# Optimization experiments

Measured on AMD Instinct MI355X. Metric: run time of the kernel, lower is better.

Reference implementation:

```python
import jax, jax.numpy as jnp
import numpy as np


def _lstm_cell(x, h, c, W_ih, b_ih, W_hh, b_hh):
    # PyTorch gate order: i, f, g, o
    gates = x @ W_ih.T + b_ih + h @ W_hh.T + b_hh
    i, f, g, o = jnp.split(gates, 4, axis=-1)
    c = jax.nn.sigmoid(f) * c + jax.nn.sigmoid(i) * jnp.tanh(g)
    h = jax.nn.sigmoid(o) * jnp.tanh(c)
    return h, c


def setup_inputs() -> dict:
    key = jax.random.key(0)
    ks = jax.random.split(key, 12)
    B, CR, PR = 8192, 168, 24
    E, I, H = 20, 3, 40  # embedding_size, input_size, hidden_size
    s = 0.1
    return {
        "z1": jax.random.normal(ks[0], (B, CR, 1), jnp.float32),
        "xc": jax.random.normal(ks[1], (B, CR + PR, I), jnp.float32),
        "W_emb": jax.random.normal(ks[2], (E, 1), jnp.float32) * s,
        "b_emb": jax.random.normal(ks[3], (E,), jnp.float32) * s,
        "W_ih": jax.random.normal(ks[4], (4 * H, E + I), jnp.float32) * s,
        "b_ih": jax.random.normal(ks[5], (4 * H,), jnp.float32) * s,
        "W_hh": jax.random.normal(ks[6], (4 * H, H), jnp.float32) * s,
        "b_hh": jax.random.normal(ks[7], (4 * H,), jnp.float32) * s,
        "W_mu": jax.random.normal(ks[8], (1, H), jnp.float32) * s,
        "b_mu": jax.random.normal(ks[9], (1,), jnp.float32) * s,
        "W_sig": jax.random.normal(ks[10], (1, H), jnp.float32) * s,
        "b_sig": jax.random.normal(ks[11], (1,), jnp.float32) * s,
        "conditioning_range": 168,
        "prediction_range": 24,
    }


def reference(z1, xc, W_emb, b_emb, W_ih, b_ih, W_hh, b_hh, W_mu, b_mu, W_sig, b_sig, conditioning_range, prediction_range):
    B = z1.shape[0]
    H = W_hh.shape[1]
    v = jnp.mean(z1, axis=1, keepdims=True) + 1.0  # [B,1,1] scale factor
    v2 = v[:, 0, :]                                # [B,1]

    # ---- conditioning phase: t = 1 .. CR-1 ----
    emb_cond = (z1[:, : conditioning_range - 1, :] / v) @ W_emb.T + b_emb  # [B,CR-1,E]
    xs = jnp.concatenate([emb_cond, xc[:, 1:conditioning_range, :]], axis=-1)
    xs = jnp.swapaxes(xs, 0, 1)  # [T,B,E+I]
    h0 = jnp.zeros((B, H), z1.dtype)
    c0 = jnp.zeros((B, H), z1.dtype)

    def cond_step(carry, x_t):
        h, c = carry
        h, c = _lstm_cell(x_t, h, c, W_ih, b_ih, W_hh, b_hh)
        return (h, c), None

    (h, c), _ = jax.lax.scan(cond_step, (h0, c0), xs)

    eps = jax.random.normal(jax.random.key(42), (prediction_range, B, 1), z1.dtype)
    xc_pred = jnp.swapaxes(
        xc[:, conditioning_range: conditioning_range + prediction_range, :], 0, 1
    )  # [PR,B,I]

    def pred_step(carry, inp):
        h, c, y = carry
        x_t, e_t = inp
        emb = (y / v2) @ W_emb.T + b_emb                       # [B,E]
        h, c = _lstm_cell(jnp.concatenate([emb, x_t], axis=-1), h, c, W_ih, b_ih, W_hh, b_hh)
        mu = h @ W_mu.T + b_mu                                 # [B,1]
        sigma = jax.nn.softplus(h @ W_sig.T + b_sig)           # [B,1]
        y = jax.lax.stop_gradient(mu + sigma * e_t)            # Normal.sample (no grad)
        return (h, c, y), (y * v2, mu * v2, sigma * v2)

    y0 = z1[:, -1, :]  # [B,1]
    _, (outs, mus, sigmas) = jax.lax.scan(pred_step, (h, c, y0), (xc_pred, eps))

    outputs = jnp.swapaxes(outs, 0, 1)[..., :]   # [B,PR,1]
    mus = jnp.swapaxes(mus, 0, 1)
    sigmas = jnp.swapaxes(sigmas, 0, 1)
    return outputs, mus, sigmas
```

## Files before the change

### kernel.cpp

```cpp
#include <hip/hip_runtime.h>

#define B_TOTAL   8192
#define CR_LEN    168
#define PR_LEN    24
#define HID       40
#define ROWS      6
#define NTHREADS  256
#define OUT_STRIDE (B_TOTAL * PR_LEN)

__device__ __forceinline__ float fast_rcp(float x) { return __builtin_amdgcn_rcpf(x); }

__device__ __forceinline__ float sigmoid_f(float x) {
    return fast_rcp(1.0f + __expf(-x));
}

__device__ __forceinline__ float tanh_f(float x) {
    float ax = fabsf(x);
    float e  = __expf(-2.0f * ax);
    float r  = (1.0f - e) * fast_rcp(1.0f + e);
    return copysignf(r, x);
}

__device__ __forceinline__ unsigned rotl32(unsigned x, int d) {
    return (x << d) | (x >> (32 - d));
}

__device__ __forceinline__ void threefry2x32(unsigned k0, unsigned k1,
                                             unsigned c0, unsigned c1,
                                             unsigned& o0, unsigned& o1) {
    const unsigned k2 = 0x1BD11BDAu ^ k0 ^ k1;
    unsigned x0 = c0 + k0, x1 = c1 + k1;
#define TF_R(rr) { x0 += x1; x1 = rotl32(x1, (rr)); x1 ^= x0; }
    TF_R(13) TF_R(15) TF_R(26) TF_R(6)  x0 += k1; x1 += k2 + 1u;
    TF_R(17) TF_R(29) TF_R(16) TF_R(24) x0 += k2; x1 += k0 + 2u;
    TF_R(13) TF_R(15) TF_R(26) TF_R(6)  x0 += k0; x1 += k1 + 3u;
    TF_R(17) TF_R(29) TF_R(16) TF_R(24) x0 += k1; x1 += k2 + 4u;
    TF_R(13) TF_R(15) TF_R(26) TF_R(6)  x0 += k2; x1 += k0 + 5u;
#undef TF_R
    o0 = x0; o1 = x1;
}

__device__ __forceinline__ float erfinv_f(float x) {
    float w = -__logf(fmaf(-x, x, 1.0f));
    float p;
    if (w < 5.0f) {
        w -= 2.5f;
        p = 2.81022636e-08f;
        p = fmaf(p, w, 3.43273939e-07f);
        p = fmaf(p, w, -3.5233877e-06f);
        p = fmaf(p, w, -4.39150654e-06f);
        p = fmaf(p, w, 0.00021858087f);
        p = fmaf(p, w, -0.00125372503f);
        p = fmaf(p, w, -0.00417768164f);
        p = fmaf(p, w, 0.246640727f);
        p = fmaf(p, w, 1.50140941f);
    } else {
        w = sqrtf(w) - 3.0f;
        p = -0.000200214257f;
        p = fmaf(p, w, 0.000100950558f);
        p = fmaf(p, w, 0.00134934322f);
        p = fmaf(p, w, -0.00367342844f);
        p = fmaf(p, w, 0.00573950773f);
        p = fmaf(p, w, -0.0076224613f);
        p = fmaf(p, w, 0.00943887047f);
        p = fmaf(p, w, 1.00167406f);
        p = fmaf(p, w, 2.83297682f);
    }
    return p * x;
}

__device__ __forceinline__ float kat_poison() {
    float poison = 0.0f;
    unsigned o0, o1;
    threefry2x32(0u, 0u, 0u, 0u, o0, o1);
    bool ok1 = (o0 == 0x6b200159u) && (o1 == 0x99ba4efeu);
    threefry2x32(0xFFFFFFFFu, 0xFFFFFFFFu, 0xFFFFFFFFu, 0xFFFFFFFFu, o0, o1);
    bool ok2 = (o0 == 0x1cb996fcu) && (o1 == 0xbb002be7u);
    if (!(ok1 && ok2)) poison += 4096.0f;
    threefry2x32(0x13198a2eu, 0x03707344u, 0x243f6a88u, 0x85a308d3u, o0, o1);
    bool ok3 = (o0 == 0xc4923a9cu) && (o1 == 0x483df7a0u);
    if (!ok3) poison += 8192.0f;
    return poison;
}

#define KEEPQ(q) asm volatile("" : "+v"((q).x), "+v"((q).y), "+v"((q).z), "+v"((q).w))

#define DOT4(acc, w4, h4) \
    acc = fmaf((w4).x, (h4).x, acc); acc = fmaf((w4).y, (h4).y, acc); \
    acc = fmaf((w4).z, (h4).z, acc); acc = fmaf((w4).w, (h4).w, acc);

#define LSTM_STEP(z1n, xa, xb, xv, hptr) do {                                  \
    float a0 = fmaf(fA0, (z1n), fC0); float a1 = fmaf(fA1, (z1n), fC1);        \
    float a2 = fmaf(fA2, (z1n), fC2); float a3 = fmaf(fA3, (z1n), fC3);        \
    a0 = fmaf(fp00, (xa), a0); a1 = fmaf(fp01, (xa), a1);                      \
    a2 = fmaf(fp02, (xa), a2); a3 = fmaf(fp03, (xa), a3);                      \
    a0 = fmaf(fp10, (xb), a0); a1 = fmaf(fp11, (xb), a1);                      \
    a2 = fmaf(fp12, (xb), a2); a3 = fmaf(fp13, (xb), a3);                      \
    a0 = fmaf(fp20, (xv), a0); a1 = fmaf(fp21, (xv), a1);                      \
    a2 = fmaf(fp22, (xv), a2); a3 = fmaf(fp23, (xv), a3);                      \
    float4 h4;                                                                 \
    h4 = ((const float4*)(hptr))[0];                                           \
    DOT4(a0, wA0, h4) DOT4(a1, wB0, h4) DOT4(a2, wC0, h4) DOT4(a3, wD0, h4)    \
    h4 = ((const float4*)(hptr))[1];                                           \
    DOT4(a0, wA1, h4) DOT4(a1, wB1, h4) DOT4(a2, wC1, h4) DOT4(a3, wD1, h4)    \
    h4 = ((const float4*)(hptr))[2];                                           \
    DOT4(a0, wA2, h4) DOT4(a1, wB2, h4) DOT4(a2, wC2, h4) DOT4(a3, wD2, h4)    \
    h4 = ((const float4*)(hptr))[3];                                           \
    DOT4(a0, wA3, h4) DOT4(a1, wB3, h4) DOT4(a2, wC3, h4) DOT4(a3, wD3, h4)    \
    h4 = ((const float4*)(hptr))[4];                                           \
    DOT4(a0, wA4, h4) DOT4(a1, wB4, h4) DOT4(a2, wC4, h4) DOT4(a3, wD4, h4)    \
    h4 = ((const float4*)(hptr))[5];                                           \
    DOT4(a0, wA5, h4) DOT4(a1, wB5, h4) DOT4(a2, wC5, h4) DOT4(a3, wD5, h4)    \
    h4 = ((const float4*)(hptr))[6];                                           \
    DOT4(a0, wA6, h4) DOT4(a1, wB6, h4) DOT4(a2, wC6, h4) DOT4(a3, wD6, h4)    \
    h4 = ((const float4*)(hptr))[7];                                           \
    DOT4(a0, wA7, h4) DOT4(a1, wB7, h4) DOT4(a2, wC7, h4) DOT4(a3, wD7, h4)    \
    h4 = ((const float4*)(hptr))[8];                                           \
    DOT4(a0, wA8, h4) DOT4(a1, wB8, h4) DOT4(a2, wC8, h4) DOT4(a3, wD8, h4)    \
    h4 = ((const float4*)(hptr))[9];                                           \
    DOT4(a0, wA9, h4) DOT4(a1, wB9, h4) DOT4(a2, wC9, h4) DOT4(a3, wD9, h4)    \
    float gi = sigmoid_f(a0);                                                  \
    float gf = sigmoid_f(a1);                                                  \
    float gg = tanh_f(a2);                                                     \
    float go = sigmoid_f(a3);                                                  \
    c_st = fmaf(gf, c_st, gi * gg);                                            \
    h_st = go * tanh_f(c_st);                                                  \
} while (0)

#define LOADW(P, base)                                                         \
    float4 P##0 = pw[(base) + 0], P##1 = pw[(base) + 1],                       \
           P##2 = pw[(base) + 2], P##3 = pw[(base) + 3],                       \
           P##4 = pw[(base) + 4], P##5 = pw[(base) + 5],                       \
           P##6 = pw[(base) + 6], P##7 = pw[(base) + 7],                       \
           P##8 = pw[(base) + 8], P##9 = pw[(base) + 9];                       \
    KEEPQ(P##0); KEEPQ(P##1); KEEPQ(P##2); KEEPQ(P##3); KEEPQ(P##4);           \
    KEEPQ(P##5); KEEPQ(P##6); KEEPQ(P##7); KEEPQ(P##8); KEEPQ(P##9);

#define XCOEF(g, fAv, fCv, f0v, f1v, f2v) {                                    \
    const int row_ = (g) * HID + j;                                            \
    const float* wr_ = W_ih + row_ * 23;                                       \
    float a_ = 0.0f, cc_ = b_ih[row_] + b_hh[row_];                            \
    _Pragma("unroll")                                                          \
    for (int e = 0; e < 20; e++) {                                             \
        float wv_ = wr_[e];                                                    \
        a_  = fmaf(wv_, W_emb[e], a_);                                         \
        cc_ = fmaf(wv_, b_emb[e], cc_);                                        \
    }                                                                          \
    fAv = a_; fCv = cc_; f0v = wr_[20]; f1v = wr_[21]; f2v = wr_[22];          \
}

__launch_bounds__(NTHREADS, 1)
__global__ void deepar_kernel(const float* __restrict__ z1,
                              const float* __restrict__ xc,
                              const float* __restrict__ W_emb,
                              const float* __restrict__ b_emb,
                              const float* __restrict__ W_ih,
                              const float* __restrict__ b_ih,
                              const float* __restrict__ W_hh,
                              const float* __restrict__ b_hh,
                              const float* __restrict__ W_mu,
                              const float* __restrict__ b_mu,
                              const float* __restrict__ W_sig,
                              const float* __restrict__ b_sig,
                              float* __restrict__ out) {
    __shared__ __align__(16) float z1_s[ROWS][CR_LEN];
    __shared__ __align__(16) float xc_s[ROWS][(CR_LEN + PR_LEN) * 3];
    __shared__ __align__(16) float h_s[2][ROWS][HID];
    __shared__ float eps_s[ROWS][PR_LEN];
    __shared__ float y_s[ROWS];
    __shared__ __align__(16) float wmu_s[HID];
    __shared__ __align__(16) float wsg_s[HID];
    __shared__ float bmu_s, bsg_s;

    const int tid = threadIdx.x;
    const int r   = tid / HID;
    const int j   = tid % HID;
    const int b0  = blockIdx.x * ROWS;
    const int b   = b0 + r;
    const bool active = (r < ROWS) && (b < B_TOTAL);

    {
        int nrow = B_TOTAL - b0;
        if (nrow > ROWS) nrow = ROWS;
        if (nrow < 0) nrow = 0;
        const float4* s1 = (const float4*)(z1 + (size_t)b0 * CR_LEN);
        float4* d1 = (float4*)&z1_s[0][0];
        const int n1 = nrow * (CR_LEN / 4);
        for (int idx = tid; idx < n1; idx += NTHREADS) d1[idx] = s1[idx];
        const float4* s2 = (const float4*)(xc + (size_t)b0 * (CR_LEN + PR_LEN) * 3);
        float4* d2 = (float4*)&xc_s[0][0];
        const int n2 = nrow * ((CR_LEN + PR_LEN) * 3 / 4);
        for (int idx = tid; idx < n2; idx += NTHREADS) d2[idx] = s2[idx];
    }
    if (tid < HID)                 wmu_s[tid] = W_mu[tid];
    else if (tid < 2 * HID)        wsg_s[tid - HID] = W_sig[tid - HID];
    else if (tid == 2 * HID)       bmu_s = b_mu[0];
    else if (tid == 2 * HID + 1)   bsg_s = b_sig[0];

    const float4* pw = (const float4*)W_hh;
    LOADW(wA, (0 * HID + j) * 10)
    LOADW(wB, (1 * HID + j) * 10)
    LOADW(wC, (2 * HID + j) * 10)
    LOADW(wD, (3 * HID + j) * 10)

    float fA0, fA1, fA2, fA3, fC0, fC1, fC2, fC3;
    float fp00, fp01, fp02, fp03, fp10, fp11, fp12, fp13, fp20, fp21, fp22, fp23;
    XCOEF(0, fA0, fC0, fp00, fp10, fp20)
    XCOEF(1, fA1, fC1, fp01, fp11, fp21)
    XCOEF(2, fA2, fC2, fp02, fp12, fp22)
    XCOEF(3, fA3, fC3, fp03, fp13, fp23)

    __syncthreads();

    float v = 0.0f, inv_v = 0.0f;
    if (active) {
        float s = 0.0f;
#pragma unroll
        for (int q = 0; q < CR_LEN / 4; q++) {
            float4 zz = *(const float4*)&z1_s[r][4 * q];
            s += zz.x + zz.y + zz.z + zz.w;
        }
        v = s * (1.0f / (float)CR_LEN) + 1.0f;
        inv_v = 1.0f / v;
    }

    if (active && j < PR_LEN) {
        unsigned i = (unsigned)j * B_TOTAL + (unsigned)b;
        unsigned o0, o1;
        threefry2x32(0u, 42u, 0u, i, o0, o1);
        unsigned bits = o0 ^ o1;
        float f = __uint_as_float((bits >> 9) | 0x3F800000u) - 1.0f;
        const float lo = -0.99999994f;
        float u = fmaxf(lo, fmaf(f, 2.0f, lo));
        eps_s[r][j] = 1.41421356237f * erfinv_f(u);
    }

    if (active) { h_s[0][r][j] = 0.0f; }
    float c_st = 0.0f, h_st = 0.0f;
    __syncthreads();

    int cur = 0;

    for (int t = 0; t < CR_LEN - 1; t++) {
        if (active) {
            float z1n = z1_s[r][t] * inv_v;
            float xa = xc_s[r][3 * (t + 1) + 0];
            float xb = xc_s[r][3 * (t + 1) + 1];
            float xv = xc_s[r][3 * (t + 1) + 2];
            LSTM_STEP(z1n, xa, xb, xv, &h_s[cur][r][0]);
            h_s[cur ^ 1][r][j] = h_st;
        }
        __syncthreads();
        cur ^= 1;
    }

    if (active && j == 0) y_s[r] = z1_s[r][CR_LEN - 1];
    __syncthreads();

    for (int t = 0; t < PR_LEN; t++) {
        if (active) {
            float z1n = y_s[r] * inv_v;
            float xa = xc_s[r][3 * (CR_LEN + t) + 0];
            float xb = xc_s[r][3 * (CR_LEN + t) + 1];
            float xv = xc_s[r][3 * (CR_LEN + t) + 2];
            LSTM_STEP(z1n, xa, xb, xv, &h_s[cur][r][0]);
            h_s[cur ^ 1][r][j] = h_st;
        }
        __syncthreads();
        cur ^= 1;
        if (active && j == 0) {
            float mu = bmu_s, sp = bsg_s;
#pragma unroll
            for (int q = 0; q < 10; q++) {
                float4 h4 = *(const float4*)&h_s[cur][r][4 * q];
                float4 wm = *(const float4*)&wmu_s[4 * q];
                float4 ws = *(const float4*)&wsg_s[4 * q];
                mu = fmaf(wm.x, h4.x, mu); mu = fmaf(wm.y, h4.y, mu);
                mu = fmaf(wm.z, h4.z, mu); mu = fmaf(wm.w, h4.w, mu);
                sp = fmaf(ws.x, h4.x, sp); sp = fmaf(ws.y, h4.y, sp);
                sp = fmaf(ws.z, h4.z, sp); sp = fmaf(ws.w, h4.w, sp);
            }
            float sigma = fmaxf(sp, 0.0f) + log1pf(__expf(-fabsf(sp)));
            float y = fmaf(sigma, eps_s[r][t], mu);
            y_s[r] = y;
            const int ob = b * PR_LEN + t;
            float poison = (b == 0 && t == 0) ? kat_poison() : 0.0f;
            out[ob]                  = y * v + poison;
            out[OUT_STRIDE + ob]     = mu * v;
            out[2 * OUT_STRIDE + ob] = sigma * v;
        }
        __syncthreads();
    }
}

extern "C" void kernel_launch(void* const* d_in, const int* in_sizes, int n_in,
                              void* d_out, int out_size, void* d_ws, size_t ws_size,
                              hipStream_t stream) {
    const float* z1    = (const float*)d_in[0];
    const float* xc    = (const float*)d_in[1];
    const float* W_emb = (const float*)d_in[2];
    const float* b_emb = (const float*)d_in[3];
    const float* W_ih  = (const float*)d_in[4];
    const float* b_ih  = (const float*)d_in[5];
    const float* W_hh  = (const float*)d_in[6];
    const float* b_hh  = (const float*)d_in[7];
    const float* W_mu  = (const float*)d_in[8];
    const float* b_mu  = (const float*)d_in[9];
    const float* W_sig = (const float*)d_in[10];
    const float* b_sig = (const float*)d_in[11];
    float* out = (float*)d_out;

    dim3 grid((B_TOTAL + ROWS - 1) / ROWS);
    dim3 block(NTHREADS);
    deepar_kernel<<<grid, block, 0, stream>>>(z1, xc, W_emb, b_emb, W_ih, b_ih,
                                              W_hh, b_hh, W_mu, b_mu, W_sig, b_sig,
                                              out);
}
```

Measured before the change: 535.7 us.

## Split LSTM gates across two thread halves with shared-memory exchange

Each hidden unit's four gates are now computed by two threads, each owning two gates (i,f vs g,o), with g/o pre-activations exchanged through shared memory. Blocks shrink to 4 batch rows with 320 threads, so each thread holds half the recurrent weights and does half the dot-product work per step. The cost is an extra __syncthreads per timestep, more blocks, and partial-batch guards removed (relies on B divisible by 4).

Result: slower. 954.0 us (+78.1%).

```diff
diff --git a/kernel.cpp b/kernel.cpp
--- a/kernel.cpp
+++ b/kernel.cpp
@@ -4,8 +4,8 @@
 #define CR_LEN    168
 #define PR_LEN    24
 #define HID       40
-#define ROWS      6
-#define NTHREADS  256
+#define ROWS      4
+#define NTHREADS  320
 #define OUT_STRIDE (B_TOTAL * PR_LEN)
 
 __device__ __forceinline__ float fast_rcp(float x) { return __builtin_amdgcn_rcpf(x); }
@@ -89,44 +89,6 @@
     acc = fmaf((w4).x, (h4).x, acc); acc = fmaf((w4).y, (h4).y, acc); \
     acc = fmaf((w4).z, (h4).z, acc); acc = fmaf((w4).w, (h4).w, acc);
 
-#define LSTM_STEP(z1n, xa, xb, xv, hptr) do {                                  \
-    float a0 = fmaf(fA0, (z1n), fC0); float a1 = fmaf(fA1, (z1n), fC1);        \
-    float a2 = fmaf(fA2, (z1n), fC2); float a3 = fmaf(fA3, (z1n), fC3);        \
-    a0 = fmaf(fp00, (xa), a0); a1 = fmaf(fp01, (xa), a1);                      \
-    a2 = fmaf(fp02, (xa), a2); a3 = fmaf(fp03, (xa), a3);                      \
-    a0 = fmaf(fp10, (xb), a0); a1 = fmaf(fp11, (xb), a1);                      \
-    a2 = fmaf(fp12, (xb), a2); a3 = fmaf(fp13, (xb), a3);                      \
-    a0 = fmaf(fp20, (xv), a0); a1 = fmaf(fp21, (xv), a1);                      \
-    a2 = fmaf(fp22, (xv), a2); a3 = fmaf(fp23, (xv), a3);                      \
-    float4 h4;                                                                 \
-    h4 = ((const float4*)(hptr))[0];                                           \
-    DOT4(a0, wA0, h4) DOT4(a1, wB0, h4) DOT4(a2, wC0, h4) DOT4(a3, wD0, h4)    \
-    h4 = ((const float4*)(hptr))[1];                                           \
-    DOT4(a0, wA1, h4) DOT4(a1, wB1, h4) DOT4(a2, wC1, h4) DOT4(a3, wD1, h4)    \
-    h4 = ((const float4*)(hptr))[2];                                           \
-    DOT4(a0, wA2, h4) DOT4(a1, wB2, h4) DOT4(a2, wC2, h4) DOT4(a3, wD2, h4)    \
-    h4 = ((const float4*)(hptr))[3];                                           \
-    DOT4(a0, wA3, h4) DOT4(a1, wB3, h4) DOT4(a2, wC3, h4) DOT4(a3, wD3, h4)    \
-    h4 = ((const float4*)(hptr))[4];                                           \
-    DOT4(a0, wA4, h4) DOT4(a1, wB4, h4) DOT4(a2, wC4, h4) DOT4(a3, wD4, h4)    \
-    h4 = ((const float4*)(hptr))[5];                                           \
-    DOT4(a0, wA5, h4) DOT4(a1, wB5, h4) DOT4(a2, wC5, h4) DOT4(a3, wD5, h4)    \
-    h4 = ((const float4*)(hptr))[6];                                           \
-    DOT4(a0, wA6, h4) DOT4(a1, wB6, h4) DOT4(a2, wC6, h4) DOT4(a3, wD6, h4)    \
-    h4 = ((const float4*)(hptr))[7];                                           \
-    DOT4(a0, wA7, h4) DOT4(a1, wB7, h4) DOT4(a2, wC7, h4) DOT4(a3, wD7, h4)    \
-    h4 = ((const float4*)(hptr))[8];                                           \
-    DOT4(a0, wA8, h4) DOT4(a1, wB8, h4) DOT4(a2, wC8, h4) DOT4(a3, wD8, h4)    \
-    h4 = ((const float4*)(hptr))[9];                                           \
-    DOT4(a0, wA9, h4) DOT4(a1, wB9, h4) DOT4(a2, wC9, h4) DOT4(a3, wD9, h4)    \
-    float gi = sigmoid_f(a0);                                                  \
-    float gf = sigmoid_f(a1);                                                  \
-    float gg = tanh_f(a2);                                                     \
-    float go = sigmoid_f(a3);                                                  \
-    c_st = fmaf(gf, c_st, gi * gg);                                            \
-    h_st = go * tanh_f(c_st);                                                  \
-} while (0)
-
 #define LOADW(P, base)                                                         \
     float4 P##0 = pw[(base) + 0], P##1 = pw[(base) + 1],                       \
            P##2 = pw[(base) + 2], P##3 = pw[(base) + 3],                       \
@@ -148,6 +110,38 @@
     }                                                                          \
     fAv = a_; fCv = cc_; f0v = wr_[20]; f1v = wr_[21]; f2v = wr_[22];          \
 }
+
+#define CELL_STEP(z1n, xa, xb, xv) do {                                        \
+    float ae = fmaf(fAe, (z1n), fCe); float af = fmaf(fAf, (z1n), fCf);        \
+    ae = fmaf(fp0e, (xa), ae); af = fmaf(fp0f, (xa), af);                      \
+    ae = fmaf(fp1e, (xb), ae); af = fmaf(fp1f, (xb), af);                      \
+    ae = fmaf(fp2e, (xv), ae); af = fmaf(fp2f, (xv), af);                      \
+    const float4* hp = (const float4*)&h_s[cur][r][0];                         \
+    float4 h4;                                                                 \
+    h4 = hp[0]; DOT4(ae, wE0, h4) DOT4(af, wF0, h4)                            \
+    h4 = hp[1]; DOT4(ae, wE1, h4) DOT4(af, wF1, h4)                            \
+    h4 = hp[2]; DOT4(ae, wE2, h4) DOT4(af, wF2, h4)                            \
+    h4 = hp[3]; DOT4(ae, wE3, h4) DOT4(af, wF3, h4)                            \
+    h4 = hp[4]; DOT4(ae, wE4, h4) DOT4(af, wF4, h4)                            \
+    h4 = hp[5]; DOT4(ae, wE5, h4) DOT4(af, wF5, h4)                            \
+    h4 = hp[6]; DOT4(ae, wE6, h4) DOT4(af, wF6, h4)                            \
+    h4 = hp[7]; DOT4(ae, wE7, h4) DOT4(af, wF7, h4)                            \
+    h4 = hp[8]; DOT4(ae, wE8, h4) DOT4(af, wF8, h4)                            \
+    h4 = hp[9]; DOT4(ae, wE9, h4) DOT4(af, wF9, h4)                            \
+    if (ph) { ex_s[r][j] = make_float2(ae, af); }                \
+    __syncthreads();                                                           \
+    if (!ph) {                                                                 \
+        float2 exgo = ex_s[r][j];                                              \
+        float gi = sigmoid_f(ae);                                              \
+        float gf = sigmoid_f(af);                                              \
+        float gg = tanh_f(exgo.x);                                             \
+        float go = sigmoid_f(exgo.y);                                          \
+        c_st = fmaf(gf, c_st, gi * gg);                                        \
+        h_s[cur ^ 1][r][j] = go * tanh_f(c_st);                                \
+    }                                                                          \
+    __syncthreads();                                                           \
+    cur ^= 1;                                                                  \
+} while (0)
 
 __launch_bounds__(NTHREADS, 1)
 __global__ void deepar_kernel(const float* __restrict__ z1,
@@ -166,6 +160,7 @@
     __shared__ __align__(16) float z1_s[ROWS][CR_LEN];
     __shared__ __align__(16) float xc_s[ROWS][(CR_LEN + PR_LEN) * 3];
     __shared__ __align__(16) float h_s[2][ROWS][HID];
+    __shared__ float2 ex_s[ROWS][HID];
     __shared__ float eps_s[ROWS][PR_LEN];
     __shared__ float y_s[ROWS];
     __shared__ __align__(16) float wmu_s[HID];
@@ -173,102 +168,80 @@
     __shared__ float bmu_s, bsg_s;
 
     const int tid = threadIdx.x;
-    const int r   = tid / HID;
-    const int j   = tid % HID;
-    const int b0  = blockIdx.x * ROWS;
-    const int b   = b0 + r;
-    const bool active = (r < ROWS) && (b < B_TOTAL);
+    const int ph  = tid / 160;
+    const int u   = tid - ph * 160;
+    const int r   = u / HID;
+    const int j   = u - r * HID;
+    const int b   = blockIdx.x * ROWS + r;
 
     {
-        int nrow = B_TOTAL - b0;
-        if (nrow > ROWS) nrow = ROWS;
-        if (nrow < 0) nrow = 0;
-        const float4* s1 = (const float4*)(z1 + (size_t)b0 * CR_LEN);
+        const float4* s1 = (const float4*)(z1 + (size_t)blockIdx.x * ROWS * CR_LEN);
         float4* d1 = (float4*)&z1_s[0][0];
-        const int n1 = nrow * (CR_LEN / 4);
-        for (int idx = tid; idx < n1; idx += NTHREADS) d1[idx] = s1[idx];
-        const float4* s2 = (const float4*)(xc + (size_t)b0 * (CR_LEN + PR_LEN) * 3);
+        for (int idx = tid; idx < ROWS * (CR_LEN / 4); idx += NTHREADS) d1[idx] = s1[idx];
+        const float4* s2 = (const float4*)(xc + (size_t)blockIdx.x * ROWS * (CR_LEN + PR_LEN) * 3);
         float4* d2 = (float4*)&xc_s[0][0];
-        const int n2 = nrow * ((CR_LEN + PR_LEN) * 3 / 4);
-        for (int idx = tid; idx < n2; idx += NTHREADS) d2[idx] = s2[idx];
+        for (int idx = tid; idx < ROWS * ((CR_LEN + PR_LEN) * 3 / 4); idx += NTHREADS) d2[idx] = s2[idx];
     }
     if (tid < HID)                 wmu_s[tid] = W_mu[tid];
     else if (tid < 2 * HID)        wsg_s[tid - HID] = W_sig[tid - HID];
     else if (tid == 2 * HID)       bmu_s = b_mu[0];
     else if (tid == 2 * HID + 1)   bsg_s = b_sig[0];
 
+    float fAe, fCe, fp0e, fp1e, fp2e;
+    float fAf, fCf, fp0f, fp1f, fp2f;
+    XCOEF(2 * ph,     fAe, fCe, fp0e, fp1e, fp2e)
+    XCOEF(2 * ph + 1, fAf, fCf, fp0f, fp1f, fp2f)
+
     const float4* pw = (const float4*)W_hh;
-    LOADW(wA, (0 * HID + j) * 10)
-    LOADW(wB, (1 * HID + j) * 10)
-    LOADW(wC, (2 * HID + j) * 10)
-    LOADW(wD, (3 * HID + j) * 10)
-
-    float fA0, fA1, fA2, fA3, fC0, fC1, fC2, fC3;
-    float fp00, fp01, fp02, fp03, fp10, fp11, fp12, fp13, fp20, fp21, fp22, fp23;
-    XCOEF(0, fA0, fC0, fp00, fp10, fp20)
-    XCOEF(1, fA1, fC1, fp01, fp11, fp21)
-    XCOEF(2, fA2, fC2, fp02, fp12, fp22)
-    XCOEF(3, fA3, fC3, fp03, fp13, fp23)
+    LOADW(wE, ((2 * ph) * HID + j) * 10)
+    LOADW(wF, ((2 * ph + 1) * HID + j) * 10)
 
     __syncthreads();
 
-    float v = 0.0f, inv_v = 0.0f;
-    if (active) {
-        float s = 0.0f;
+    float s = 0.0f;
 #pragma unroll
-        for (int q = 0; q < CR_LEN / 4; q++) {
-            float4 zz = *(const float4*)&z1_s[r][4 * q];
-            s += zz.x + zz.y + zz.z + zz.w;
-        }
-        v = s * (1.0f / (float)CR_LEN) + 1.0f;
-        inv_v = 1.0f / v;
-    }
-
-    if (active && j < PR_LEN) {
+    for (int q = 0; q < CR_LEN / 4; q++) {
+        float4 zz = *(const float4*)&z1_s[r][4 * q];
+        s += zz.x + zz.y + zz.z + zz.w;
+    }
+    const float v = s * (1.0f / (float)CR_LEN) + 1.0f;
+    const float inv_v = 1.0f / v;
+
+    if (ph == 0 && j < PR_LEN) {
         unsigned i = (unsigned)j * B_TOTAL + (unsigned)b;
         unsigned o0, o1;
         threefry2x32(0u, 42u, 0u, i, o0, o1);
         unsigned bits = o0 ^ o1;
         float f = __uint_as_float((bits >> 9) | 0x3F800000u) - 1.0f;
         const float lo = -0.99999994f;
-        float u = fmaxf(lo, fmaf(f, 2.0f, lo));
-        eps_s[r][j] = 1.41421356237f * erfinv_f(u);
-    }
-
-    if (active) { h_s[0][r][j] = 0.0f; }
-    float c_st = 0.0f, h_st = 0.0f;
+        float uu = fmaxf(lo, fmaf(f, 2.0f, lo));
+        eps_s[r][j] = 1.41421356237f * erfinv_f(uu);
+    }
+
+    if (ph == 0) h_s[0][r][j] = 0.0f;
+    float c_st = 0.0f;
     __syncthreads();
 
     int cur = 0;
 
     for (int t = 0; t < CR_LEN - 1; t++) {
-        if (active) {
-            float z1n = z1_s[r][t] * inv_v;
-            float xa = xc_s[r][3 * (t + 1) + 0];
-            float xb = xc_s[r][3 * (t + 1) + 1];
-            float xv = xc_s[r][3 * (t + 1) + 2];
-            LSTM_STEP(z1n, xa, xb, xv, &h_s[cur][r][0]);
-            h_s[cur ^ 1][r][j] = h_st;
-        }
-        __syncthreads();
-        cur ^= 1;
-    }
-
-    if (active && j == 0) y_s[r] = z1_s[r][CR_LEN - 1];
+        float z1n = z1_s[r][t] * inv_v;
+        float xa = xc_s[r][3 * (t + 1) + 0];
+        float xb = xc_s[r][3 * (t + 1) + 1];
+        float xv = xc_s[r][3 * (t + 1) + 2];
+        CELL_STEP(z1n, xa, xb, xv);
+    }
+
+    if (ph == 0 && j == 0) y_s[r] = z1_s[r][CR_LEN - 1];
     __syncthreads();
 
     for (int t = 0; t < PR_LEN; t++) {
-        if (active) {
-            float z1n = y_s[r] * inv_v;
-            float xa = xc_s[r][3 * (CR_LEN + t) + 0];
-            float xb = xc_s[r][3 * (CR_LEN + t) + 1];
-            float xv = xc_s[r][3 * (CR_LEN + t) + 2];
-            LSTM_STEP(z1n, xa, xb, xv, &h_s[cur][r][0]);
-            h_s[cur ^ 1][r][j] = h_st;
-        }
-        __syncthreads();
-        cur ^= 1;
-        if (active && j == 0) {
+        float z1n = y_s[r] * inv_v;
+        float xa = xc_s[r][3 * (CR_LEN + t) + 0];
+        float xb = xc_s[r][3 * (CR_LEN + t) + 1];
+        float xv = xc_s[r][3 * (CR_LEN + t) + 2];
+        CELL_STEP(z1n, xa, xb, xv);
+        if (ph == 0 && j == 0) {
             float mu = bmu_s, sp = bsg_s;
 #pragma unroll
             for (int q = 0; q < 10; q++) {
@@ -310,7 +283,7 @@
     const float* b_sig = (const float*)d_in[11];
     float* out = (float*)d_out;
 
-    dim3 grid((B_TOTAL + ROWS - 1) / ROWS);
+    dim3 grid(B_TOTAL / ROWS);
     dim3 block(NTHREADS);
     deepar_kernel<<<grid, block, 0, stream>>>(z1, xc, W_emb, b_emb, W_ih, b_ih,
                                               W_hh, b_hh, W_mu, b_mu, W_sig, b_sig,
```
